# Performance work log

Measured on AMD Instinct MI355X. Metric: run time of the kernel, lower is better.

Reference implementation:

```python
import jax, jax.numpy as jnp
import numpy as np

EMB = 1024
NH = 16
T = 2048
B = 2

def setup_inputs() -> dict:
    key = jax.random.key(0)
    k1, k2, k3, k4, k5 = jax.random.split(key, 5)
    s = 0.02
    return {
        "x": jax.random.normal(k1, (B, T, EMB), dtype=jnp.float32),
        "W_attn": jax.random.normal(k2, (EMB, 3 * EMB), dtype=jnp.float32) * s,
        "b_attn": jax.random.normal(k3, (3 * EMB,), dtype=jnp.float32) * s,
        "W_proj": jax.random.normal(k4, (EMB, EMB), dtype=jnp.float32) * s,
        "b_proj": jax.random.normal(k5, (EMB,), dtype=jnp.float32) * s,
    }

def reference(x, W_attn, b_attn, W_proj, b_proj):
    Bz, Tz, C = x.shape
    hd = C // NH
    qkv = x @ W_attn + b_attn                      # [B,T,3C]
    q, k, v = jnp.split(qkv, 3, axis=-1)
    # [B,T,C] -> [B,H,T,hd]
    def heads(t):
        return t.reshape(Bz, Tz, NH, hd).transpose(0, 2, 1, 3)
    q, k, v = heads(q), heads(k), heads(v)
    scale = 1.0 / jnp.sqrt(jnp.float32(hd))
    att = jnp.einsum("bhqd,bhkd->bhqk", q, k) * scale   # [B,H,T,T]
    causal = jnp.tril(jnp.ones((Tz, Tz), dtype=bool))
    att = jnp.where(causal, att, jnp.finfo(att.dtype).min)
    att = jax.nn.softmax(att, axis=-1)
    y = jnp.einsum("bhqk,bhkd->bhqd", att, v)            # [B,H,T,hd]
    y = y.transpose(0, 2, 1, 3).reshape(Bz, Tz, C)
    return y @ W_proj + b_proj
```

## Files before the change

kernel.cpp:

```cpp
#include <hip/hip_runtime.h>
#include <cstdint>
#include <cstddef>

typedef _Float16 half8 __attribute__((ext_vector_type(8)));
typedef _Float16 half4v __attribute__((ext_vector_type(4)));
typedef float f32x4 __attribute__((ext_vector_type(4)));
typedef int int4v __attribute__((ext_vector_type(4)));

#define EMBD 1024
#define NHEAD 16
#define TSEQ 2048
#define NB 2
#define HD 64
#define NBH (NB*NHEAD)
#define SCK 0.18033688f

static __device__ __forceinline__ void gload_lds16(const void* g, void* l) {
    __builtin_amdgcn_global_load_lds((const __attribute__((address_space(1))) void*)g,
                                     (__attribute__((address_space(3))) void*)l,
                                     16, 0, 0);
}

static __device__ __forceinline__ int pk2(float a, float b) {
    return __builtin_bit_cast(int, __builtin_amdgcn_cvt_pkrtz(a, b));
}

__global__ void k_convert_x(const float* __restrict__ x, _Float16* __restrict__ xh, int n4) {
    int i = blockIdx.x * blockDim.x + threadIdx.x;
    if (i < n4) {
        float4 v = ((const float4*)x)[i];
        half4v h;
        h.x = (_Float16)v.x; h.y = (_Float16)v.y; h.z = (_Float16)v.z; h.w = (_Float16)v.w;
        ((half4v*)xh)[i] = h;
    }
}

__global__ void k_prep_w(const float* __restrict__ Wa, const float* __restrict__ Wp,
                         _Float16* __restrict__ WaT, _Float16* __restrict__ WpT) {
    __shared__ float tile[32][33];
    const int bx = blockIdx.x;
    const bool isA = bx < 96;
    const float* in  = isA ? Wa : Wp;
    _Float16* out    = isA ? WaT : WpT;
    const int C      = isA ? 3072 : 1024;
    const int c0 = (isA ? bx : bx - 96) * 32, r0 = blockIdx.y * 32;
    const int tx = threadIdx.x, ty = threadIdx.y;
    #pragma unroll
    for (int j = 0; j < 4; ++j)
        tile[ty + 8*j][tx] = in[(size_t)(r0 + ty + 8*j) * C + c0 + tx];
    __syncthreads();
    #pragma unroll
    for (int j = 0; j < 4; ++j)
        out[(size_t)(c0 + ty + 8*j) * 1024 + r0 + tx] = (_Float16)tile[tx][ty + 8*j];
}

__global__ __launch_bounds__(256) void k_gemm_qkv(
    const _Float16* __restrict__ A,
    const _Float16* __restrict__ Bt,
    const float* __restrict__ bias,
    _Float16* __restrict__ outq,
    _Float16* __restrict__ VT)
{
    __shared__ _Float16 smem[16512];
    _Float16* As = smem;
    _Float16* Bs = smem + 8192;

    const int d  = blockIdx.x;
    const int wk = (d & 7) * 96 + (d >> 3);
    const int mt = wk & 31, nt = wk >> 5;
    const int m0 = mt * 128, n0 = nt * 128;

    const int tid  = threadIdx.x;
    const int lane = tid & 63;
    const int w    = tid >> 6;
    const int wm   = w >> 1, wn = w & 1;
    const int l15  = lane & 15;
    const int lg   = lane >> 4;

    const int srow  = lane >> 3;
    const int sslot = (lane & 7) ^ srow;

    f32x4 acc[4][4];
    #pragma unroll
    for (int i = 0; i < 4; ++i)
        #pragma unroll
        for (int j = 0; j < 4; ++j)
            acc[i][j] = (f32x4){0.f, 0.f, 0.f, 0.f};

    for (int kt = 0; kt < 16; ++kt) {
        __syncthreads();
        #pragma unroll
        for (int c = 0; c < 4; ++c) {
            int r = w * 32 + c * 8 + srow;
            const _Float16* ga = A  + (size_t)(m0 + r) * 1024 + kt * 64 + sslot * 8;
            gload_lds16(ga, (char*)As + (w * 32 + c * 8) * 128);
            const _Float16* gb = Bt + (size_t)(n0 + r) * 1024 + kt * 64 + sslot * 8;
            gload_lds16(gb, (char*)Bs + (w * 32 + c * 8) * 128);
        }
        __syncthreads();

        half8 af[4][2], bf[4][2];
        #pragma unroll
        for (int mf = 0; mf < 4; ++mf) {
            int r = wm * 64 + mf * 16 + l15;
            #pragma unroll
            for (int ks = 0; ks < 2; ++ks)
                af[mf][ks] = *(const half8*)((const char*)As + r * 128 + (((ks * 4 + lg) ^ (r & 7)) * 16));
        }
        #pragma unroll
        for (int nf = 0; nf < 4; ++nf) {
            int r = wn * 64 + nf * 16 + l15;
            #pragma unroll
            for (int ks = 0; ks < 2; ++ks)
                bf[nf][ks] = *(const half8*)((const char*)Bs + r * 128 + (((ks * 4 + lg) ^ (r & 7)) * 16));
        }
        #pragma unroll
        for (int mf = 0; mf < 4; ++mf)
            #pragma unroll
            for (int nf = 0; nf < 4; ++nf) {
                acc[mf][nf] = __builtin_amdgcn_mfma_f32_16x16x32_f16(af[mf][0], bf[nf][0], acc[mf][nf], 0, 0, 0);
                acc[mf][nf] = __builtin_amdgcn_mfma_f32_16x16x32_f16(af[mf][1], bf[nf][1], acc[mf][nf], 0, 0, 0);
            }
    }

    float bv[4];
    #pragma unroll
    for (int nf = 0; nf < 4; ++nf)
        bv[nf] = bias[n0 + wn * 64 + nf * 16 + l15];

    const int which = n0 >> 10;
    if (which < 2) {
        const float osc = (which == 1) ? SCK : 1.0f;
        #pragma unroll
        for (int mf = 0; mf < 4; ++mf) {
            #pragma unroll
            for (int j = 0; j < 4; ++j) {
                int m = m0 + wm * 64 + mf * 16 + lg * 4 + j;
                _Float16* po = outq + (size_t)m * 3072 + n0 + wn * 64 + l15;
                #pragma unroll
                for (int nf = 0; nf < 4; ++nf)
                    po[nf * 16] = (_Float16)((acc[mf][nf][j] + bv[nf]) * osc);
            }
        }
    } else {
        __syncthreads();
        #pragma unroll
        for (int mf = 0; mf < 4; ++mf)
            #pragma unroll
            for (int j = 0; j < 4; ++j) {
                int m = wm * 64 + mf * 16 + lg * 4 + j;
                #pragma unroll
                for (int nf = 0; nf < 4; ++nf) {
                    int n = wn * 64 + nf * 16 + l15;
                    smem[m * 129 + n] = (_Float16)(acc[mf][nf][j] + bv[nf]);
                }
            }
        __syncthreads();

        const int b     = m0 >> 11;
        const int h0    = (n0 - 2048) >> 6;
        const int tloc0 = m0 & 2047;
        #pragma unroll
        for (int c = 0; c < 8; ++c) {
            int seg = c * 256 + tid;
            int hd  = seg >> 4;
            int s   = seg & 15;
            half8 hv8;
            #pragma unroll
            for (int e = 0; e < 8; ++e) {
                int p = s * 8 + e;
                int k = 16 * (2 * (p >> 5) + ((p & 7) >> 2)) + 4 * ((p >> 3) & 3) + (p & 3);
                hv8[e] = smem[k * 129 + hd];
            }
            size_t row = (size_t)(b * 16 + h0 + (hd >> 6)) * 64 + (hd & 63);
            *(half8*)&VT[row * 2048 + tloc0 + s * 8] = hv8;
        }
    }
}

__global__ __launch_bounds__(256) void k_gemm_proj(
    const _Float16* __restrict__ A,
    const _Float16* __restrict__ Bt,
    const float* __restrict__ bias,
    float* __restrict__ outf)
{
    __shared__ _Float16 As[64 * 64];
    __shared__ _Float16 Bs[128 * 64];

    const int d  = blockIdx.x;
    const int wk = (d & 7) * 64 + (d >> 3);
    const int mt = wk & 63, nt = wk >> 6;
    const int m0 = mt * 64, n0 = nt * 128;

    const int tid  = threadIdx.x;
    const int lane = tid & 63;
    const int wn   = tid >> 6;
    const int l15  = lane & 15;
    const int lg   = lane >> 4;

    f32x4 acc[4][2];
    #pragma unroll
    for (int i = 0; i < 4; ++i) {
        acc[i][0] = (f32x4){0.f, 0.f, 0.f, 0.f};
        acc[i][1] = (f32x4){0.f, 0.f, 0.f, 0.f};
    }

    for (int kt = 0; kt < 16; ++kt) {
        __syncthreads();
        #pragma unroll
        for (int c = 0; c < 2; ++c) {
            int s = c * 256 + tid;
            int r = s >> 3, sl = s & 7;
            const _Float16* ga = A + (size_t)(m0 + r) * 1024 + kt * 64 + ((sl ^ (r & 7)) * 8);
            gload_lds16(ga, (char*)As + s * 16);
        }
        #pragma unroll
        for (int c = 0; c < 4; ++c) {
            int s = c * 256 + tid;
            int r = s >> 3, sl = s & 7;
            const _Float16* gb = Bt + (size_t)(n0 + r) * 1024 + kt * 64 + ((sl ^ (r & 7)) * 8);
            gload_lds16(gb, (char*)Bs + s * 16);
        }
        __syncthreads();

        half8 af[4][2], bf[2][2];
        #pragma unroll
        for (int mf = 0; mf < 4; ++mf) {
            int r = mf * 16 + l15;
            #pragma unroll
            for (int ks = 0; ks < 2; ++ks)
                af[mf][ks] = *(const half8*)((const char*)As + r * 128 + (((ks * 4 + lg) ^ (r & 7)) * 16));
        }
        #pragma unroll
        for (int nf = 0; nf < 2; ++nf) {
            int r = wn * 32 + nf * 16 + l15;
            #pragma unroll
            for (int ks = 0; ks < 2; ++ks)
                bf[nf][ks] = *(const half8*)((const char*)Bs + r * 128 + (((ks * 4 + lg) ^ (r & 7)) * 16));
        }
        #pragma unroll
        for (int mf = 0; mf < 4; ++mf)
            #pragma unroll
            for (int nf = 0; nf < 2; ++nf) {
                acc[mf][nf] = __builtin_amdgcn_mfma_f32_16x16x32_f16(af[mf][0], bf[nf][0], acc[mf][nf], 0, 0, 0);
                acc[mf][nf] = __builtin_amdgcn_mfma_f32_16x16x32_f16(af[mf][1], bf[nf][1], acc[mf][nf], 0, 0, 0);
            }
    }

    float bv[2];
    bv[0] = bias[n0 + wn * 32 + l15];
    bv[1] = bias[n0 + wn * 32 + 16 + l15];

    #pragma unroll
    for (int mf = 0; mf < 4; ++mf) {
        #pragma unroll
        for (int j = 0; j < 4; ++j) {
            int m = m0 + mf * 16 + lg * 4 + j;
            float* po = outf + (size_t)m * 1024 + n0 + wn * 32 + l15;
            po[0]  = acc[mf][0][j] + bv[0];
            po[16] = acc[mf][1][j] + bv[1];
        }
    }
}

__global__ __launch_bounds__(512) void k_attn(
    const _Float16* __restrict__ qkv,
    const _Float16* __restrict__ VTg,
    _Float16* __restrict__ Y)
{
    __shared__ _Float16 Kt[128 * 64];
    __shared__ _Float16 Vt[64 * 128];

    const int tid  = threadIdx.x;
    const int lane = tid & 63;
    const int w    = tid >> 6;
    const int l15  = lane & 15;
    const int lg   = lane >> 4;
    const int bh   = blockIdx.x;
    const int by   = blockIdx.y;
    const int qt   = (by < 8) ? (15 - by) : (by - 8);
    const int b    = bh >> 4, h = bh & 15;

    const int rA  = tid >> 3;
    const int slA = tid & 7;
    const size_t kOffA = (size_t)rA * 3072 + ((slA ^ (rA & 7)) * 8);
    const _Float16* kBase = qkv + (size_t)(b * 2048) * 3072 + 1024 + h * 64;

    const int dA = tid >> 4;
    const int sA = tid & 15;
    const size_t vOffA = (size_t)dA * 2048 + ((sA ^ (dA & 15)) * 8);
    const _Float16* vBase = VTg + (size_t)bh * TSEQ * HD;

    const int x7   = l15 & 7;
    const int kph0 = (lg ^ x7) * 8;
    const int kph1 = ((4 + lg) ^ x7) * 8;

    const int qrow = qt * 128 + w * 16 + l15;
    const _Float16* qptr = qkv + (size_t)(b * 2048 + qrow) * 3072 + h * 64;
    half8 qa0 = *(const half8*)&qptr[lg * 8];
    half8 qa1 = *(const half8*)&qptr[32 + lg * 8];

    half8 ones;
    #pragma unroll
    for (int i = 0; i < 8; ++i) ones[i] = (_Float16)1.0f;

    f32x4 yac[4];
    #pragma unroll
    for (int nf = 0; nf < 4; ++nf) yac[nf] = (f32x4){0.f, 0.f, 0.f, 0.f};
    f32x4 lsum = (f32x4){0.f, 0.f, 0.f, 0.f};

    const int nkt = qt + 1;

    half8 kra = *(const half8*)(kBase + kOffA);
    half8 krb = *(const half8*)(kBase + kOffA + (size_t)64 * 3072);
    half8 vra = *(const half8*)(vBase + vOffA);
    half8 vrb = *(const half8*)(vBase + vOffA + 32 * 2048);

    for (int kt = 0; kt < nkt; ++kt) {
        __syncthreads();
        *(half8*)&Kt[tid * 8]        = kra;
        *(half8*)&Kt[4096 + tid * 8] = krb;
        *(half8*)&Vt[tid * 8]        = vra;
        *(half8*)&Vt[4096 + tid * 8] = vrb;
        if (kt + 1 < nkt) {
            const _Float16* kp = kBase + (size_t)(kt + 1) * 128 * 3072;
            kra = *(const half8*)(kp + kOffA);
            krb = *(const half8*)(kp + kOffA + (size_t)64 * 3072);
            const _Float16* vp = vBase + (kt + 1) * 128;
            vra = *(const half8*)(vp + vOffA);
            vrb = *(const half8*)(vp + vOffA + 32 * 2048);
        }
        __syncthreads();

        const bool diag = (kt == nkt - 1);

        f32x4 s[8];
        __builtin_amdgcn_s_setprio(1);
        #pragma unroll
        for (int f = 0; f < 8; ++f) {
            if (diag && f > w) { s[f] = (f32x4){0.f, 0.f, 0.f, 0.f}; continue; }
            int rr = f * 16 + l15;
            half8 kb0 = *(const half8*)&Kt[rr * 64 + kph0];
            half8 kb1 = *(const half8*)&Kt[rr * 64 + kph1];
            f32x4 z = (f32x4){0.f, 0.f, 0.f, 0.f};
            z = __builtin_amdgcn_mfma_f32_16x16x32_f16(kb0, qa0, z, 0, 0, 0);
            z = __builtin_amdgcn_mfma_f32_16x16x32_f16(kb1, qa1, z, 0, 0, 0);
            s[f] = z;
        }
        __builtin_amdgcn_s_setprio(0);

        if (diag) {
            const int qg = qt * 128 + w * 16 + l15;
            #pragma unroll
            for (int f = 0; f < 8; ++f) {
                if (f > w) continue;
                #pragma unroll
                for (int j = 0; j < 4; ++j) {
                    int kk = kt * 128 + 16 * f + 4 * lg + j;
                    s[f][j] = (kk > qg) ? 0.f : exp2f(s[f][j]);
                }
            }
        } else {
            #pragma unroll
            for (int f = 0; f < 8; ++f)
                #pragma unroll
                for (int j = 0; j < 4; ++j) s[f][j] = exp2f(s[f][j]);
        }

        __builtin_amdgcn_s_setprio(1);
        #pragma unroll
        for (int t = 0; t < 4; ++t) {
            int4v pi;
            pi[0] = pk2(s[2 * t][0],     s[2 * t][1]);
            pi[1] = pk2(s[2 * t][2],     s[2 * t][3]);
            pi[2] = pk2(s[2 * t + 1][0], s[2 * t + 1][1]);
            pi[3] = pk2(s[2 * t + 1][2], s[2 * t + 1][3]);
            half8 pa = __builtin_bit_cast(half8, pi);
            lsum = __builtin_amdgcn_mfma_f32_16x16x32_f16(pa, ones, lsum, 0, 0, 0);
            #pragma unroll
            for (int nf = 0; nf < 4; ++nf) {
                half8 vb = *(const half8*)&Vt[(nf * 16 + l15) * 128 + (((t * 4 + lg) ^ l15) * 8)];
                yac[nf] = __builtin_amdgcn_mfma_f32_16x16x32_f16(pa, vb, yac[nf], 0, 0, 0);
            }
        }
        __builtin_amdgcn_s_setprio(0);
    }

    const int trow = qt * 128 + w * 16 + lg * 4;
    #pragma unroll
    for (int j = 0; j < 4; ++j) {
        float inv = 1.f / lsum[j];
        #pragma unroll
        for (int nf = 0; nf < 4; ++nf) {
            float yv = yac[nf][j] * inv;
            Y[((size_t)b * TSEQ + trow + j) * EMBD + h * 64 + nf * 16 + l15] = (_Float16)yv;
        }
    }
}

extern "C" void kernel_launch(void* const* d_in, const int* in_sizes, int n_in,
                              void* d_out, int out_size, void* d_ws, size_t ws_size,
                              hipStream_t stream) {
    const float* x  = (const float*)d_in[0];
    const float* Wa = (const float*)d_in[1];
    const float* ba = (const float*)d_in[2];
    const float* Wp = (const float*)d_in[3];
    const float* bp = (const float*)d_in[4];
    float* out = (float*)d_out;

    _Float16* Xh   = (_Float16*)d_ws;
    _Float16* WaT  = Xh   + (size_t)4096 * 1024;
    _Float16* WpT  = WaT  + (size_t)3072 * 1024;
    _Float16* QKVn = WpT  + (size_t)1024 * 1024;
    _Float16* VTb  = QKVn + (size_t)4096 * 3072;
    _Float16* Yh   = Xh;

    k_convert_x<<<4096, 256, 0, stream>>>(x, Xh, 1048576);
    k_prep_w<<<dim3(128, 32), dim3(32, 8), 0, stream>>>(Wa, Wp, WaT, WpT);

    k_gemm_qkv<<<768, 256, 0, stream>>>(Xh, WaT, ba, QKVn, VTb);

    k_attn<<<dim3(NBH, 16), 512, 0, stream>>>(QKVn, VTb, Yh);

    k_gemm_proj<<<512, 256, 0, stream>>>(Yh, WpT, bp, out);
}
```

Measured before the change: 110.8 us.

## Shrink QKV GEMM tile to 128x64, remap blocks per XCD, fuse prep kernels

The QKV GEMM tile drops from 128x128 to 128x64, so the grid doubles to 1536 blocks with smaller accumulators and less LDS per block. Blocks are remapped so each XCD covers a contiguous region of M and N tiles, and the projection GEMM gets the same kind of L2-friendly mapping. The x conversion and weight transpose kernels are merged into one launch to save a kernel launch. The smaller tile raises occupancy but lowers reuse of each loaded A tile, which increases A-operand traffic.

```diff
diff --git a/kernel.cpp b/kernel.cpp
--- a/kernel.cpp
+++ b/kernel.cpp
@@ -25,26 +25,30 @@
     return __builtin_bit_cast(int, __builtin_amdgcn_cvt_pkrtz(a, b));
 }
 
-__global__ void k_convert_x(const float* __restrict__ x, _Float16* __restrict__ xh, int n4) {
-    int i = blockIdx.x * blockDim.x + threadIdx.x;
-    if (i < n4) {
+__global__ __launch_bounds__(256) void k_prep(
+    const float* __restrict__ x,  _Float16* __restrict__ xh,
+    const float* __restrict__ Wa, const float* __restrict__ Wp,
+    _Float16* __restrict__ WaT,   _Float16* __restrict__ WpT)
+{
+    const int bx = blockIdx.x;
+    if (bx < 4096) {
+        int i = bx * 256 + threadIdx.x;
         float4 v = ((const float4*)x)[i];
         half4v h;
         h.x = (_Float16)v.x; h.y = (_Float16)v.y; h.z = (_Float16)v.z; h.w = (_Float16)v.w;
         ((half4v*)xh)[i] = h;
-    }
-}
-
-__global__ void k_prep_w(const float* __restrict__ Wa, const float* __restrict__ Wp,
-                         _Float16* __restrict__ WaT, _Float16* __restrict__ WpT) {
+        return;
+    }
     __shared__ float tile[32][33];
-    const int bx = blockIdx.x;
-    const bool isA = bx < 96;
+    const int idx = bx - 4096;
+    const int bxx = idx & 127;
+    const int byy = idx >> 7;
+    const bool isA = bxx < 96;
     const float* in  = isA ? Wa : Wp;
     _Float16* out    = isA ? WaT : WpT;
     const int C      = isA ? 3072 : 1024;
-    const int c0 = (isA ? bx : bx - 96) * 32, r0 = blockIdx.y * 32;
-    const int tx = threadIdx.x, ty = threadIdx.y;
+    const int c0 = (isA ? bxx : bxx - 96) * 32, r0 = byy * 32;
+    const int tx = threadIdx.x & 31, ty = threadIdx.x >> 5;
     #pragma unroll
     for (int j = 0; j < 4; ++j)
         tile[ty + 8*j][tx] = in[(size_t)(r0 + ty + 8*j) * C + c0 + tx];
@@ -61,14 +65,16 @@
     _Float16* __restrict__ outq,
     _Float16* __restrict__ VT)
 {
-    __shared__ _Float16 smem[16512];
+    __shared__ _Float16 smem[12288];
     _Float16* As = smem;
     _Float16* Bs = smem + 8192;
 
-    const int d  = blockIdx.x;
-    const int wk = (d & 7) * 96 + (d >> 3);
-    const int mt = wk & 31, nt = wk >> 5;
-    const int m0 = mt * 128, n0 = nt * 128;
+    const int d    = blockIdx.x;
+    const int xcd  = d & 7;
+    const int idx  = d >> 3;
+    const int mt   = (xcd >> 1) * 8  + (idx & 7);
+    const int ntl  = (xcd &  1) * 24 + (idx >> 3);
+    const int m0 = mt * 128, n0 = ntl * 64;
 
     const int tid  = threadIdx.x;
     const int lane = tid & 63;
@@ -77,29 +83,32 @@
     const int l15  = lane & 15;
     const int lg   = lane >> 4;
 
-    const int srow  = lane >> 3;
-    const int sslot = (lane & 7) ^ srow;
-
-    f32x4 acc[4][4];
-    #pragma unroll
-    for (int i = 0; i < 4; ++i)
-        #pragma unroll
-        for (int j = 0; j < 4; ++j)
-            acc[i][j] = (f32x4){0.f, 0.f, 0.f, 0.f};
+    f32x4 acc[4][2];
+    #pragma unroll
+    for (int i = 0; i < 4; ++i) {
+        acc[i][0] = (f32x4){0.f, 0.f, 0.f, 0.f};
+        acc[i][1] = (f32x4){0.f, 0.f, 0.f, 0.f};
+    }
 
     for (int kt = 0; kt < 16; ++kt) {
         __syncthreads();
         #pragma unroll
         for (int c = 0; c < 4; ++c) {
-            int r = w * 32 + c * 8 + srow;
-            const _Float16* ga = A  + (size_t)(m0 + r) * 1024 + kt * 64 + sslot * 8;
-            gload_lds16(ga, (char*)As + (w * 32 + c * 8) * 128);
-            const _Float16* gb = Bt + (size_t)(n0 + r) * 1024 + kt * 64 + sslot * 8;
-            gload_lds16(gb, (char*)Bs + (w * 32 + c * 8) * 128);
-        }
-        __syncthreads();
-
-        half8 af[4][2], bf[4][2];
+            int s = c * 256 + tid;
+            int r = s >> 3, sl = s & 7;
+            const _Float16* ga = A + (size_t)(m0 + r) * 1024 + kt * 64 + ((sl ^ (r & 7)) * 8);
+            gload_lds16(ga, (char*)As + s * 16);
+        }
+        #pragma unroll
+        for (int c = 0; c < 2; ++c) {
+            int s = c * 256 + tid;
+            int r = s >> 3, sl = s & 7;
+            const _Float16* gb = Bt + (size_t)(n0 + r) * 1024 + kt * 64 + ((sl ^ (r & 7)) * 8);
+            gload_lds16(gb, (char*)Bs + s * 16);
+        }
+        __syncthreads();
+
+        half8 af[4][2], bf[2][2];
         #pragma unroll
         for (int mf = 0; mf < 4; ++mf) {
             int r = wm * 64 + mf * 16 + l15;
@@ -108,8 +117,8 @@
                 af[mf][ks] = *(const half8*)((const char*)As + r * 128 + (((ks * 4 + lg) ^ (r & 7)) * 16));
         }
         #pragma unroll
-        for (int nf = 0; nf < 4; ++nf) {
-            int r = wn * 64 + nf * 16 + l15;
+        for (int nf = 0; nf < 2; ++nf) {
+            int r = wn * 32 + nf * 16 + l15;
             #pragma unroll
             for (int ks = 0; ks < 2; ++ks)
                 bf[nf][ks] = *(const half8*)((const char*)Bs + r * 128 + (((ks * 4 + lg) ^ (r & 7)) * 16));
@@ -117,16 +126,15 @@
         #pragma unroll
         for (int mf = 0; mf < 4; ++mf)
             #pragma unroll
-            for (int nf = 0; nf < 4; ++nf) {
+            for (int nf = 0; nf < 2; ++nf) {
                 acc[mf][nf] = __builtin_amdgcn_mfma_f32_16x16x32_f16(af[mf][0], bf[nf][0], acc[mf][nf], 0, 0, 0);
                 acc[mf][nf] = __builtin_amdgcn_mfma_f32_16x16x32_f16(af[mf][1], bf[nf][1], acc[mf][nf], 0, 0, 0);
             }
     }
 
-    float bv[4];
-    #pragma unroll
-    for (int nf = 0; nf < 4; ++nf)
-        bv[nf] = bias[n0 + wn * 64 + nf * 16 + l15];
+    float bv[2];
+    bv[0] = bias[n0 + wn * 32 + l15];
+    bv[1] = bias[n0 + wn * 32 + 16 + l15];
 
     const int which = n0 >> 10;
     if (which < 2) {
@@ -136,10 +144,9 @@
             #pragma unroll
             for (int j = 0; j < 4; ++j) {
                 int m = m0 + wm * 64 + mf * 16 + lg * 4 + j;
-                _Float16* po = outq + (size_t)m * 3072 + n0 + wn * 64 + l15;
-                #pragma unroll
-                for (int nf = 0; nf < 4; ++nf)
-                    po[nf * 16] = (_Float16)((acc[mf][nf][j] + bv[nf]) * osc);
+                _Float16* po = outq + (size_t)m * 3072 + n0 + wn * 32 + l15;
+                po[0]  = (_Float16)((acc[mf][0][j] + bv[0]) * osc);
+                po[16] = (_Float16)((acc[mf][1][j] + bv[1]) * osc);
             }
         }
     } else {
@@ -149,31 +156,28 @@
             #pragma unroll
             for (int j = 0; j < 4; ++j) {
                 int m = wm * 64 + mf * 16 + lg * 4 + j;
-                #pragma unroll
-                for (int nf = 0; nf < 4; ++nf) {
-                    int n = wn * 64 + nf * 16 + l15;
-                    smem[m * 129 + n] = (_Float16)(acc[mf][nf][j] + bv[nf]);
-                }
+                smem[m * 65 + wn * 32 + l15]      = (_Float16)(acc[mf][0][j] + bv[0]);
+                smem[m * 65 + wn * 32 + 16 + l15] = (_Float16)(acc[mf][1][j] + bv[1]);
             }
         __syncthreads();
 
         const int b     = m0 >> 11;
-        const int h0    = (n0 - 2048) >> 6;
+        const int h     = (n0 - 2048) >> 6;
         const int tloc0 = m0 & 2047;
-        #pragma unroll
-        for (int c = 0; c < 8; ++c) {
+        _Float16* vbase = VT + ((size_t)(b * 16 + h) * 64) * 2048 + tloc0;
+        #pragma unroll
+        for (int c = 0; c < 4; ++c) {
             int seg = c * 256 + tid;
-            int hd  = seg >> 4;
+            int dd  = seg >> 4;
             int s   = seg & 15;
             half8 hv8;
             #pragma unroll
             for (int e = 0; e < 8; ++e) {
                 int p = s * 8 + e;
                 int k = 16 * (2 * (p >> 5) + ((p & 7) >> 2)) + 4 * ((p >> 3) & 3) + (p & 3);
-                hv8[e] = smem[k * 129 + hd];
-            }
-            size_t row = (size_t)(b * 16 + h0 + (hd >> 6)) * 64 + (hd & 63);
-            *(half8*)&VT[row * 2048 + tloc0 + s * 8] = hv8;
+                hv8[e] = smem[k * 65 + dd];
+            }
+            *(half8*)&vbase[(size_t)dd * 2048 + s * 8] = hv8;
         }
     }
 }
@@ -187,9 +191,11 @@
     __shared__ _Float16 As[64 * 64];
     __shared__ _Float16 Bs[128 * 64];
 
-    const int d  = blockIdx.x;
-    const int wk = (d & 7) * 64 + (d >> 3);
-    const int mt = wk & 63, nt = wk >> 6;
+    const int d   = blockIdx.x;
+    const int xcd = d & 7;
+    const int idx = d >> 3;
+    const int mt  = (xcd >> 1) * 16 + (idx & 15);
+    const int nt  = (xcd &  1) * 4  + (idx >> 4);
     const int m0 = mt * 64, n0 = nt * 128;
 
     const int tid  = threadIdx.x;
@@ -415,10 +421,9 @@
     _Float16* VTb  = QKVn + (size_t)4096 * 3072;
     _Float16* Yh   = Xh;
 
-    k_convert_x<<<4096, 256, 0, stream>>>(x, Xh, 1048576);
-    k_prep_w<<<dim3(128, 32), dim3(32, 8), 0, stream>>>(Wa, Wp, WaT, WpT);
-
-    k_gemm_qkv<<<768, 256, 0, stream>>>(Xh, WaT, ba, QKVn, VTb);
+    k_prep<<<8192, 256, 0, stream>>>(x, Xh, Wa, Wp, WaT, WpT);
+
+    k_gemm_qkv<<<1536, 256, 0, stream>>>(Xh, WaT, ba, QKVn, VTb);
 
     k_attn<<<dim3(NBH, 16), 512, 0, stream>>>(QKVn, VTb, Yh);
 
```

After: 97.04 us. -12.5%, faster.
